# Kernel tuning notes

Hardware: AMD Instinct MI355X
Metric: run time of the kernel (lower is better)

The kernel has to match this reference:

```python
import jax, jax.numpy as jnp
import numpy as np

EPS = 1e-12  # clamp for sqrt stability in Gram-matrix distance

def _pairwise_euclid(X, Y):
    # [B,D],[M,D] -> [B,M] Euclidean distances via Gram trick (avoids [B,M,D] diff tensor)
    x2 = jnp.sum(X * X, axis=-1, keepdims=True)        # [B,1]
    y2 = jnp.sum(Y * Y, axis=-1)[None, :]              # [1,M]
    sq = x2 + y2 - 2.0 * (X @ Y.T)
    return jnp.sqrt(jnp.maximum(sq, EPS))

def setup_inputs() -> dict:
    key = jax.random.key(0)
    k1, k2, k3 = jax.random.split(key, 3)
    B, D = 4096, 128
    return {
        "rep_anchor": jax.random.normal(k1, (B, D), dtype=jnp.float32),
        "rep_pos": jax.random.normal(k2, (B, D), dtype=jnp.float32),
        "rep_neg": jax.random.normal(k3, (B, D), dtype=jnp.float32),
    }

def reference(rep_anchor, rep_pos, rep_neg):
    B = rep_anchor.shape[0]
    # distance_pos[i] = ||a_i - p_i||_2 (elementwise rows, like F.pairwise_distance)
    diff = rep_anchor - rep_pos
    distance_pos = jnp.sqrt(jnp.maximum(jnp.sum(diff * diff, axis=-1), EPS))  # [B]

    big = jnp.asarray(jnp.finfo(rep_anchor.dtype).max, rep_anchor.dtype)
    eye = jnp.eye(B, dtype=bool)
    # anchor-as-negative: exclude self (index i)
    d_aa = jnp.where(eye, big, _pairwise_euclid(rep_anchor, rep_anchor))  # [B,B]
    # pos-as-negative: rep_pos[i] is excluded for anchor i
    d_ap = jnp.where(eye, big, _pairwise_euclid(rep_anchor, rep_pos))    # [B,B]
    # all of rep_neg are negatives
    d_an = _pairwise_euclid(rep_anchor, rep_neg)                          # [B,B]

    hardest_neg = jnp.minimum(jnp.minimum(d_aa.min(axis=1), d_ap.min(axis=1)), d_an.min(axis=1))  # [B]
    # log1p(exp(x)) == softplus, computed stably
    loss_in_batch = jnp.logaddexp(0.0, distance_pos - hardest_neg)
    return jnp.mean(loss_in_batch)
```

## Files before the change

kernel.cpp:

```cpp
#include <hip/hip_runtime.h>
#include <math.h>

#define BDIM 4096
#define DDIM 128
#define EPSF 1e-12f
#define TI 128
#define TJ 64
#define NSPLIT 16
#define NSLICE (NSPLIT * 2)
#define ITILES (BDIM / TI)
#define JT 12
#define FLT_BIG 3.402823466e+38f
#define NCHUNK (16 * BDIM)

typedef __attribute__((ext_vector_type(8))) _Float16 f16x8;
typedef __attribute__((ext_vector_type(16))) float f32x16;

__device__ __forceinline__ void gload_lds16(const void* g, void* l) {
    __builtin_amdgcn_global_load_lds(
        (const __attribute__((address_space(1))) unsigned int*)(uintptr_t)g,
        (__attribute__((address_space(3))) unsigned int*)(unsigned int)(uintptr_t)l,
        16, 0, 0);
}

__device__ __forceinline__ unsigned int pack2h(float x, float y) {
    _Float16 hx = (_Float16)x, hy = (_Float16)y;
    unsigned short ux, uy;
    __builtin_memcpy(&ux, &hx, 2);
    __builtin_memcpy(&uy, &hy, 2);
    return (unsigned int)ux | ((unsigned int)uy << 16);
}

__global__ __launch_bounds__(256) void prep_kernel(
    const float* __restrict__ A, const float* __restrict__ P,
    const float* __restrict__ N, uint4* __restrict__ Xp,
    float* __restrict__ a2, float* __restrict__ p2,
    float* __restrict__ n2, float* __restrict__ dpos) {
    int gid = blockIdx.x * 256 + threadIdx.x;
    int sl = gid & 15;
    int row = gid >> 4;
    const float4 a0 = *(const float4*)&A[row * DDIM + sl * 8];
    const float4 a1 = *(const float4*)&A[row * DDIM + sl * 8 + 4];
    const float4 p0 = *(const float4*)&P[row * DDIM + sl * 8];
    const float4 p1 = *(const float4*)&P[row * DDIM + sl * 8 + 4];
    const float4 n0 = *(const float4*)&N[row * DDIM + sl * 8];
    const float4 n1 = *(const float4*)&N[row * DDIM + sl * 8 + 4];
    uint4 ca = {pack2h(a0.x, a0.y), pack2h(a0.z, a0.w),
                pack2h(a1.x, a1.y), pack2h(a1.z, a1.w)};
    uint4 cp = {pack2h(p0.x, p0.y), pack2h(p0.z, p0.w),
                pack2h(p1.x, p1.y), pack2h(p1.z, p1.w)};
    uint4 cn = {pack2h(n0.x, n0.y), pack2h(n0.z, n0.w),
                pack2h(n1.x, n1.y), pack2h(n1.z, n1.w)};
    Xp[(0 * 16 + sl) * BDIM + row] = ca;
    Xp[(1 * 16 + sl) * BDIM + row] = cp;
    Xp[(2 * 16 + sl) * BDIM + row] = cn;
    float sa = a0.x*a0.x + a0.y*a0.y + a0.z*a0.z + a0.w*a0.w
             + a1.x*a1.x + a1.y*a1.y + a1.z*a1.z + a1.w*a1.w;
    float sp = p0.x*p0.x + p0.y*p0.y + p0.z*p0.z + p0.w*p0.w
             + p1.x*p1.x + p1.y*p1.y + p1.z*p1.z + p1.w*p1.w;
    float sn = n0.x*n0.x + n0.y*n0.y + n0.z*n0.z + n0.w*n0.w
             + n1.x*n1.x + n1.y*n1.y + n1.z*n1.z + n1.w*n1.w;
    float d0 = a0.x-p0.x, d1 = a0.y-p0.y, d2 = a0.z-p0.z, d3 = a0.w-p0.w;
    float d4 = a1.x-p1.x, d5 = a1.y-p1.y, d6 = a1.z-p1.z, d7 = a1.w-p1.w;
    float sd = d0*d0 + d1*d1 + d2*d2 + d3*d3 + d4*d4 + d5*d5 + d6*d6 + d7*d7;
    #pragma unroll
    for (int off = 1; off < 16; off <<= 1) {
        sa += __shfl_xor(sa, off);
        sp += __shfl_xor(sp, off);
        sn += __shfl_xor(sn, off);
        sd += __shfl_xor(sd, off);
    }
    if (sl == 0) {
        a2[row] = sa;
        p2[row] = sp;
        n2[row] = sn;
        dpos[row] = sqrtf(fmaxf(sd, EPSF));
    }
}

__global__ __launch_bounds__(256, 2) void minsq_kernel(
    const ushort* __restrict__ Xp,
    const float* __restrict__ a2, const float* __restrict__ p2,
    const float* __restrict__ n2, float* __restrict__ partial) {
    __shared__ __align__(16) ushort pool[4][2][4096];

    const int tid = threadIdx.x;
    const int w = tid >> 6;
    const int lane = tid & 63;
    const int rg = w >> 1;
    const int ch = w & 1;
    const int iTile = blockIdx.x;
    const int split = blockIdx.y;
    const int i0 = iTile * TI;
    const int jt0 = split * JT;
    const int l31 = lane & 31;
    const int lhi = lane >> 5;
    ushort* const wbase = &pool[w][0][0];

    {
        int jt = jt0, m = jt >> 6, tc = jt & 63;
        int rowB = tc * TJ + ch * 32 + l31;
        #pragma unroll
        for (int k = 0; k < 8; ++k) {
            int slB = k * 2 + lhi;
            gload_lds16(Xp + (size_t)((m * 16 + slB) * BDIM + rowB) * 8,
                        wbase + k * 512);
        }
    }
    f16x8 a0[8], a1[8];
    {
        int rowA0 = i0 + rg * 64 + l31;
        #pragma unroll
        for (int t = 0; t < 8; ++t) {
            int slA = t * 2 + lhi;
            a0[t] = *(const f16x8*)(Xp + (size_t)(slA * BDIM + rowA0) * 8);
            a1[t] = *(const f16x8*)(Xp + (size_t)(slA * BDIM + rowA0 + 32) * 8);
        }
    }
    float y2h[JT];
    #pragma unroll
    for (int t = 0; t < JT; ++t) {
        int jt = jt0 + t, m = jt >> 6, tc = jt & 63;
        const float* y2g = (m == 0) ? a2 : ((m == 1) ? p2 : n2);
        y2h[t] = 0.5f * y2g[tc * TJ + ch * 32 + l31];
    }
    asm volatile("s_waitcnt vmcnt(0)" ::: "memory");
    __builtin_amdgcn_sched_barrier(0);

    float minv[2][16];
    #pragma unroll
    for (int rb = 0; rb < 2; ++rb)
        #pragma unroll
        for (int g = 0; g < 16; ++g) minv[rb][g] = FLT_BIG;

    #pragma unroll
    for (int idx = 0; idx < JT; ++idx) {
        if (idx + 1 < JT) {
            int jn = jt0 + idx + 1, mn = jn >> 6, tcn = jn & 63;
            int rowB = tcn * TJ + ch * 32 + l31;
            ushort* dst = wbase + ((idx + 1) & 1) * 4096;
            #pragma unroll
            for (int k = 0; k < 8; ++k) {
                int slB = k * 2 + lhi;
                gload_lds16(Xp + (size_t)((mn * 16 + slB) * BDIM + rowB) * 8,
                            dst + k * 512);
            }
            asm volatile("s_waitcnt vmcnt(8)" ::: "memory");
        } else {
            asm volatile("s_waitcnt vmcnt(0)" ::: "memory");
        }
        __builtin_amdgcn_sched_barrier(0);

        const ushort* buf = wbase + (idx & 1) * 4096;
        f32x16 acc0 = {}, acc1 = {};
        __builtin_amdgcn_s_setprio(1);
        #pragma unroll
        for (int t = 0; t < 8; ++t) {
            f16x8 b = *(const f16x8*)&buf[t * 512 + lane * 8];
            acc0 = __builtin_amdgcn_mfma_f32_32x32x16_f16(a0[t], b, acc0, 0, 0, 0);
            acc1 = __builtin_amdgcn_mfma_f32_32x32x16_f16(a1[t], b, acc1, 0, 0, 0);
        }
        __builtin_amdgcn_s_setprio(0);

        {
            int jt = jt0 + idx, m = jt >> 6, tc = jt & 63;
            float yh = y2h[idx];
            if (m < 2 && (tc >> 1) == iTile) {
                int jg = tc * TJ + ch * 32 + l31;
                #pragma unroll
                for (int rb = 0; rb < 2; ++rb) {
                    #pragma unroll
                    for (int g = 0; g < 16; ++g) {
                        int rloc = (g & 3) + 8 * (g >> 2) + 4 * lhi;
                        int ig = i0 + rg * 64 + rb * 32 + rloc;
                        float d = (rb == 0) ? acc0[g] : acc1[g];
                        float cand = yh - d;
                        if (ig == jg) cand = FLT_BIG;
                        minv[rb][g] = fminf(minv[rb][g], cand);
                    }
                }
            } else {
                #pragma unroll
                for (int g = 0; g < 16; ++g) {
                    minv[0][g] = fminf(minv[0][g], yh - acc0[g]);
                    minv[1][g] = fminf(minv[1][g], yh - acc1[g]);
                }
            }
        }
    }

    #pragma unroll
    for (int off = 1; off < 32; off <<= 1) {
        #pragma unroll
        for (int rb = 0; rb < 2; ++rb)
            #pragma unroll
            for (int g = 0; g < 16; ++g)
                minv[rb][g] = fminf(minv[rb][g], __shfl_xor(minv[rb][g], off));
    }
    if (l31 == 0) {
        int slice = split * 2 + ch;
        #pragma unroll
        for (int rb = 0; rb < 2; ++rb) {
            #pragma unroll
            for (int g = 0; g < 16; ++g) {
                int rloc = (g & 3) + 8 * (g >> 2) + 4 * lhi;
                int ig = i0 + rg * 64 + rb * 32 + rloc;
                partial[(size_t)ig * NSLICE + slice] = minv[rb][g];
            }
        }
    }
}

__global__ __launch_bounds__(256) void lossA_kernel(
    const float* __restrict__ partial, const float* __restrict__ a2,
    const float* __restrict__ dpos, float* __restrict__ bsum) {
    __shared__ float red[4];
    int i = blockIdx.x * 256 + threadIdx.x;
    const float4* pr = (const float4*)&partial[(size_t)i * NSLICE];
    float mv = FLT_BIG;
    #pragma unroll
    for (int q = 0; q < NSLICE / 4; ++q) {
        float4 v = pr[q];
        mv = fminf(mv, fminf(fminf(v.x, v.y), fminf(v.z, v.w)));
    }
    float h2 = a2[i] + 2.0f * mv;
    float hardest = sqrtf(fmaxf(h2, EPSF));
    float x = dpos[i] - hardest;
    float sum = fmaxf(x, 0.f) + log1pf(expf(-fabsf(x)));
    #pragma unroll
    for (int off = 32; off; off >>= 1) sum += __shfl_down(sum, off);
    if ((threadIdx.x & 63) == 0) red[threadIdx.x >> 6] = sum;
    __syncthreads();
    if (threadIdx.x == 0)
        bsum[blockIdx.x] = red[0] + red[1] + red[2] + red[3];
}

__global__ void lossB_kernel(const float* __restrict__ bsum,
                             float* __restrict__ out) {
    float v = (threadIdx.x < 16) ? bsum[threadIdx.x] : 0.f;
    #pragma unroll
    for (int off = 32; off; off >>= 1) v += __shfl_down(v, off);
    if (threadIdx.x == 0) out[0] = v * (1.0f / BDIM);
}

extern "C" void kernel_launch(void* const* d_in, const int* in_sizes, int n_in,
                              void* d_out, int out_size, void* d_ws, size_t ws_size,
                              hipStream_t stream) {
    const float* A = (const float*)d_in[0];
    const float* P = (const float*)d_in[1];
    const float* N = (const float*)d_in[2];

    float* ws = (float*)d_ws;
    float* a2 = ws;
    float* p2 = ws + BDIM;
    float* n2 = ws + 2 * BDIM;
    float* dpos = ws + 3 * BDIM;
    float* bsum = ws + 4 * BDIM;
    float* partial = ws + 4 * BDIM + 64;
    uint4* Xp = (uint4*)(partial + (size_t)BDIM * NSLICE);

    prep_kernel<<<256, 256, 0, stream>>>(A, P, N, Xp, a2, p2, n2, dpos);
    dim3 grid2(ITILES, NSPLIT);
    minsq_kernel<<<grid2, 256, 0, stream>>>((const ushort*)Xp, a2, p2, n2, partial);
    lossA_kernel<<<16, 256, 0, stream>>>(partial, a2, dpos, bsum);
    lossB_kernel<<<1, 64, 0, stream>>>(bsum, (float*)d_out);
}
```

Measured before the change: 36.00 us.

## Share block-wide LDS Y tile across waves and rebalance split grid

Each wave used to stage its own copy of the B tile in LDS. Now the four waves cooperatively load one shared double-buffered 64-row tile, with block barriers to keep the buffers in sync. This cuts redundant global-to-LDS traffic and LDS footprint in half, which should allow more resident blocks. The grid split also changes from 16 splits of 12 tiles to 24 splits of 8 tiles, giving more blocks but adding partial-min slices and per-iteration barrier costs.

```diff
diff --git a/kernel.cpp b/kernel.cpp
--- a/kernel.cpp
+++ b/kernel.cpp
@@ -6,12 +6,11 @@
 #define EPSF 1e-12f
 #define TI 128
 #define TJ 64
-#define NSPLIT 16
+#define NSPLIT 24
 #define NSLICE (NSPLIT * 2)
 #define ITILES (BDIM / TI)
-#define JT 12
+#define JT 8
 #define FLT_BIG 3.402823466e+38f
-#define NCHUNK (16 * BDIM)
 
 typedef __attribute__((ext_vector_type(8))) _Float16 f16x8;
 typedef __attribute__((ext_vector_type(16))) float f32x16;
@@ -82,131 +81,129 @@
     const ushort* __restrict__ Xp,
     const float* __restrict__ a2, const float* __restrict__ p2,
     const float* __restrict__ n2, float* __restrict__ partial) {
-    __shared__ __align__(16) ushort pool[4][2][4096];
+    __shared__ __align__(16) ushort Y[2][TJ * DDIM / 1];
 
     const int tid = threadIdx.x;
     const int w = tid >> 6;
     const int lane = tid & 63;
+    const int l31 = lane & 31;
+    const int lhi = lane >> 5;
     const int rg = w >> 1;
     const int ch = w & 1;
     const int iTile = blockIdx.x;
     const int split = blockIdx.y;
     const int i0 = iTile * TI;
     const int jt0 = split * JT;
-    const int l31 = lane & 31;
-    const int lhi = lane >> 5;
-    ushort* const wbase = &pool[w][0][0];
 
     {
-        int jt = jt0, m = jt >> 6, tc = jt & 63;
-        int rowB = tc * TJ + ch * 32 + l31;
-        #pragma unroll
-        for (int k = 0; k < 8; ++k) {
-            int slB = k * 2 + lhi;
-            gload_lds16(Xp + (size_t)((m * 16 + slB) * BDIM + rowB) * 8,
-                        wbase + k * 512);
+        int m = jt0 >> 6, tc = jt0 & 63;
+        #pragma unroll
+        for (int q = 0; q < 4; ++q) {
+            int sl = w * 4 + q;
+            gload_lds16(Xp + (size_t)((m * 16 + sl) * BDIM + tc * TJ + lane) * 8,
+                        (ushort*)&Y[0][0] + sl * 512);
         }
     }
     f16x8 a0[8], a1[8];
     {
-        int rowA0 = i0 + rg * 64 + l31;
+        int rowA = i0 + rg * 64 + l31;
         #pragma unroll
         for (int t = 0; t < 8; ++t) {
-            int slA = t * 2 + lhi;
-            a0[t] = *(const f16x8*)(Xp + (size_t)(slA * BDIM + rowA0) * 8);
-            a1[t] = *(const f16x8*)(Xp + (size_t)(slA * BDIM + rowA0 + 32) * 8);
-        }
-    }
-    float y2h[JT];
-    #pragma unroll
-    for (int t = 0; t < JT; ++t) {
-        int jt = jt0 + t, m = jt >> 6, tc = jt & 63;
+            int sl = t * 2 + lhi;
+            a0[t] = *(const f16x8*)(Xp + (size_t)(sl * BDIM + rowA) * 8);
+            a1[t] = *(const f16x8*)(Xp + (size_t)(sl * BDIM + rowA + 32) * 8);
+        }
+    }
+    float y2buf[2];
+    {
+        int m = jt0 >> 6, tc = jt0 & 63;
         const float* y2g = (m == 0) ? a2 : ((m == 1) ? p2 : n2);
-        y2h[t] = 0.5f * y2g[tc * TJ + ch * 32 + l31];
+        y2buf[0] = 0.5f * y2g[tc * TJ + ch * 32 + l31];
     }
     asm volatile("s_waitcnt vmcnt(0)" ::: "memory");
     __builtin_amdgcn_sched_barrier(0);
-
-    float minv[2][16];
-    #pragma unroll
-    for (int rb = 0; rb < 2; ++rb)
-        #pragma unroll
-        for (int g = 0; g < 16; ++g) minv[rb][g] = FLT_BIG;
-
-    #pragma unroll
-    for (int idx = 0; idx < JT; ++idx) {
-        if (idx + 1 < JT) {
-            int jn = jt0 + idx + 1, mn = jn >> 6, tcn = jn & 63;
-            int rowB = tcn * TJ + ch * 32 + l31;
-            ushort* dst = wbase + ((idx + 1) & 1) * 4096;
+    __builtin_amdgcn_s_barrier();
+    __builtin_amdgcn_sched_barrier(0);
+
+    float minv0[16], minv1[16];
+    #pragma unroll
+    for (int g = 0; g < 16; ++g) { minv0[g] = FLT_BIG; minv1[g] = FLT_BIG; }
+
+    #pragma unroll
+    for (int t = 0; t < JT; ++t) {
+        if (t + 1 < JT) {
+            int jn = jt0 + t + 1, mn = jn >> 6, tcn = jn & 63;
             #pragma unroll
-            for (int k = 0; k < 8; ++k) {
-                int slB = k * 2 + lhi;
-                gload_lds16(Xp + (size_t)((mn * 16 + slB) * BDIM + rowB) * 8,
-                            dst + k * 512);
+            for (int q = 0; q < 4; ++q) {
+                int sl = w * 4 + q;
+                gload_lds16(Xp + (size_t)((mn * 16 + sl) * BDIM + tcn * TJ + lane) * 8,
+                            (ushort*)&Y[(t + 1) & 1][0] + sl * 512);
             }
-            asm volatile("s_waitcnt vmcnt(8)" ::: "memory");
+            const float* y2g = (mn == 0) ? a2 : ((mn == 1) ? p2 : n2);
+            y2buf[(t + 1) & 1] = 0.5f * y2g[tcn * TJ + ch * 32 + l31];
+            asm volatile("s_waitcnt vmcnt(5)" ::: "memory");
         } else {
             asm volatile("s_waitcnt vmcnt(0)" ::: "memory");
         }
         __builtin_amdgcn_sched_barrier(0);
-
-        const ushort* buf = wbase + (idx & 1) * 4096;
+        __builtin_amdgcn_s_barrier();
+        __builtin_amdgcn_sched_barrier(0);
+
+        const ushort* buf = &Y[t & 1][0];
         f32x16 acc0 = {}, acc1 = {};
         __builtin_amdgcn_s_setprio(1);
         #pragma unroll
-        for (int t = 0; t < 8; ++t) {
-            f16x8 b = *(const f16x8*)&buf[t * 512 + lane * 8];
-            acc0 = __builtin_amdgcn_mfma_f32_32x32x16_f16(a0[t], b, acc0, 0, 0, 0);
-            acc1 = __builtin_amdgcn_mfma_f32_32x32x16_f16(a1[t], b, acc1, 0, 0, 0);
+        for (int k = 0; k < 8; ++k) {
+            int sl = k * 2 + lhi;
+            f16x8 b = *(const f16x8*)&buf[(sl * 64 + ch * 32 + l31) * 8];
+            acc0 = __builtin_amdgcn_mfma_f32_32x32x16_f16(a0[k], b, acc0, 0, 0, 0);
+            acc1 = __builtin_amdgcn_mfma_f32_32x32x16_f16(a1[k], b, acc1, 0, 0, 0);
         }
         __builtin_amdgcn_s_setprio(0);
 
         {
-            int jt = jt0 + idx, m = jt >> 6, tc = jt & 63;
-            float yh = y2h[idx];
+            int jt = jt0 + t, m = jt >> 6, tc = jt & 63;
+            float yh = y2buf[t & 1];
             if (m < 2 && (tc >> 1) == iTile) {
                 int jg = tc * TJ + ch * 32 + l31;
                 #pragma unroll
-                for (int rb = 0; rb < 2; ++rb) {
-                    #pragma unroll
-                    for (int g = 0; g < 16; ++g) {
-                        int rloc = (g & 3) + 8 * (g >> 2) + 4 * lhi;
-                        int ig = i0 + rg * 64 + rb * 32 + rloc;
-                        float d = (rb == 0) ? acc0[g] : acc1[g];
-                        float cand = yh - d;
-                        if (ig == jg) cand = FLT_BIG;
-                        minv[rb][g] = fminf(minv[rb][g], cand);
-                    }
+                for (int g = 0; g < 16; ++g) {
+                    int rloc = (g & 3) + 8 * (g >> 2) + 4 * lhi;
+                    int ig0 = i0 + rg * 64 + rloc;
+                    float c0 = yh - acc0[g];
+                    if (ig0 == jg) c0 = FLT_BIG;
+                    minv0[g] = fminf(minv0[g], c0);
+                    float c1 = yh - acc1[g];
+                    if (ig0 + 32 == jg) c1 = FLT_BIG;
+                    minv1[g] = fminf(minv1[g], c1);
                 }
             } else {
                 #pragma unroll
                 for (int g = 0; g < 16; ++g) {
-                    minv[0][g] = fminf(minv[0][g], yh - acc0[g]);
-                    minv[1][g] = fminf(minv[1][g], yh - acc1[g]);
+                    minv0[g] = fminf(minv0[g], yh - acc0[g]);
+                    minv1[g] = fminf(minv1[g], yh - acc1[g]);
                 }
             }
         }
+        __builtin_amdgcn_s_barrier();
     }
 
     #pragma unroll
     for (int off = 1; off < 32; off <<= 1) {
         #pragma unroll
-        for (int rb = 0; rb < 2; ++rb)
-            #pragma unroll
-            for (int g = 0; g < 16; ++g)
-                minv[rb][g] = fminf(minv[rb][g], __shfl_xor(minv[rb][g], off));
+        for (int g = 0; g < 16; ++g) {
+            minv0[g] = fminf(minv0[g], __shfl_xor(minv0[g], off));
+            minv1[g] = fminf(minv1[g], __shfl_xor(minv1[g], off));
+        }
     }
     if (l31 == 0) {
         int slice = split * 2 + ch;
         #pragma unroll
-        for (int rb = 0; rb < 2; ++rb) {
-            #pragma unroll
-            for (int g = 0; g < 16; ++g) {
-                int rloc = (g & 3) + 8 * (g >> 2) + 4 * lhi;
-                int ig = i0 + rg * 64 + rb * 32 + rloc;
-                partial[(size_t)ig * NSLICE + slice] = minv[rb][g];
-            }
+        for (int g = 0; g < 16; ++g) {
+            int rloc = (g & 3) + 8 * (g >> 2) + 4 * lhi;
+            int ig = i0 + rg * 64 + rloc;
+            partial[(size_t)ig * NSLICE + slice] = minv0[g];
+            partial[(size_t)(ig + 32) * NSLICE + slice] = minv1[g];
         }
     }
 }
```

After: 36.94 us. +2.6%, slower.

## Fold column norm bias into MFMA, shrink cross-lane reduction, widen loss reduction

Applied to the files above, without the earlier changes.

Each column's -0.5*||y||^2 is stored as a two-term fp16 split, so one extra MFMA per accumulator adds the bias directly. The epilogue becomes a plain running max with no per-element subtract. The in-wave shuffle reduction drops from 5 steps to 2, and more partial slices (256 per row) are written for the loss kernel to reduce wave-wide. The loss kernel now uses 64 blocks with one wave per row group. This trades per-element ALU and shuffle work for two extra MFMAs per tile and more partial-buffer traffic, and the fp16-split bias may slightly change precision.

```diff
diff --git a/kernel.cpp b/kernel.cpp
--- a/kernel.cpp
+++ b/kernel.cpp
@@ -7,14 +7,14 @@
 #define TI 128
 #define TJ 64
 #define NSPLIT 16
-#define NSLICE (NSPLIT * 2)
+#define NSLICE 256
 #define ITILES (BDIM / TI)
 #define JT 12
 #define FLT_BIG 3.402823466e+38f
-#define NCHUNK (16 * BDIM)
 
 typedef __attribute__((ext_vector_type(8))) _Float16 f16x8;
 typedef __attribute__((ext_vector_type(16))) float f32x16;
+union VU { uint4 u; f16x8 v; };
 
 __device__ __forceinline__ void gload_lds16(const void* g, void* l) {
     __builtin_amdgcn_global_load_lds(
@@ -34,8 +34,8 @@
 __global__ __launch_bounds__(256) void prep_kernel(
     const float* __restrict__ A, const float* __restrict__ P,
     const float* __restrict__ N, uint4* __restrict__ Xp,
-    float* __restrict__ a2, float* __restrict__ p2,
-    float* __restrict__ n2, float* __restrict__ dpos) {
+    unsigned int* __restrict__ y2c, float* __restrict__ a2,
+    float* __restrict__ dpos) {
     int gid = blockIdx.x * 256 + threadIdx.x;
     int sl = gid & 15;
     int row = gid >> 4;
@@ -72,33 +72,40 @@
     }
     if (sl == 0) {
         a2[row] = sa;
-        p2[row] = sp;
-        n2[row] = sn;
         dpos[row] = sqrtf(fmaxf(sd, EPSF));
+        float ya = 0.5f * sa, yp = 0.5f * sp, yn = 0.5f * sn;
+        float ha = (float)(_Float16)ya, hp = (float)(_Float16)yp,
+              hn = (float)(_Float16)yn;
+        y2c[0 * BDIM + row] = pack2h(-ha, -(ya - ha));
+        y2c[1 * BDIM + row] = pack2h(-hp, -(yp - hp));
+        y2c[2 * BDIM + row] = pack2h(-hn, -(yn - hn));
     }
 }
 
 __global__ __launch_bounds__(256, 2) void minsq_kernel(
-    const ushort* __restrict__ Xp,
-    const float* __restrict__ a2, const float* __restrict__ p2,
-    const float* __restrict__ n2, float* __restrict__ partial) {
+    const ushort* __restrict__ Xp, const unsigned int* __restrict__ y2c,
+    float* __restrict__ partial) {
     __shared__ __align__(16) ushort pool[4][2][4096];
 
     const int tid = threadIdx.x;
     const int w = tid >> 6;
     const int lane = tid & 63;
+    const int l31 = lane & 31;
+    const int lhi = lane >> 5;
     const int rg = w >> 1;
     const int ch = w & 1;
     const int iTile = blockIdx.x;
     const int split = blockIdx.y;
     const int i0 = iTile * TI;
     const int jt0 = split * JT;
-    const int l31 = lane & 31;
-    const int lhi = lane >> 5;
     ushort* const wbase = &pool[w][0][0];
 
+    VU au; au.u = (uint4){lhi == 0 ? 0x3C003C00u : 0u, 0u, 0u, 0u};
+    const f16x8 ax = au.v;
+
+    unsigned int yc_cur, yc_nxt;
     {
-        int jt = jt0, m = jt >> 6, tc = jt & 63;
+        int m = jt0 >> 6, tc = jt0 & 63;
         int rowB = tc * TJ + ch * 32 + l31;
         #pragma unroll
         for (int k = 0; k < 8; ++k) {
@@ -106,32 +113,24 @@
             gload_lds16(Xp + (size_t)((m * 16 + slB) * BDIM + rowB) * 8,
                         wbase + k * 512);
         }
+        yc_cur = y2c[m * BDIM + rowB];
     }
     f16x8 a0[8], a1[8];
     {
-        int rowA0 = i0 + rg * 64 + l31;
+        int rowA = i0 + rg * 64 + l31;
         #pragma unroll
         for (int t = 0; t < 8; ++t) {
             int slA = t * 2 + lhi;
-            a0[t] = *(const f16x8*)(Xp + (size_t)(slA * BDIM + rowA0) * 8);
-            a1[t] = *(const f16x8*)(Xp + (size_t)(slA * BDIM + rowA0 + 32) * 8);
-        }
-    }
-    float y2h[JT];
-    #pragma unroll
-    for (int t = 0; t < JT; ++t) {
-        int jt = jt0 + t, m = jt >> 6, tc = jt & 63;
-        const float* y2g = (m == 0) ? a2 : ((m == 1) ? p2 : n2);
-        y2h[t] = 0.5f * y2g[tc * TJ + ch * 32 + l31];
+            a0[t] = *(const f16x8*)(Xp + (size_t)(slA * BDIM + rowA) * 8);
+            a1[t] = *(const f16x8*)(Xp + (size_t)(slA * BDIM + rowA + 32) * 8);
+        }
     }
     asm volatile("s_waitcnt vmcnt(0)" ::: "memory");
     __builtin_amdgcn_sched_barrier(0);
 
-    float minv[2][16];
-    #pragma unroll
-    for (int rb = 0; rb < 2; ++rb)
-        #pragma unroll
-        for (int g = 0; g < 16; ++g) minv[rb][g] = FLT_BIG;
+    float maxv0[16], maxv1[16];
+    #pragma unroll
+    for (int g = 0; g < 16; ++g) { maxv0[g] = -FLT_BIG; maxv1[g] = -FLT_BIG; }
 
     #pragma unroll
     for (int idx = 0; idx < JT; ++idx) {
@@ -145,15 +144,22 @@
                 gload_lds16(Xp + (size_t)((mn * 16 + slB) * BDIM + rowB) * 8,
                             dst + k * 512);
             }
-            asm volatile("s_waitcnt vmcnt(8)" ::: "memory");
+            yc_nxt = y2c[mn * BDIM + rowB];
+            __builtin_amdgcn_sched_barrier(0);
+            asm volatile("s_waitcnt vmcnt(9)" ::: "memory");
         } else {
             asm volatile("s_waitcnt vmcnt(0)" ::: "memory");
         }
         __builtin_amdgcn_sched_barrier(0);
+
+        VU bu; bu.u = (uint4){yc_cur, 0u, 0u, 0u};
+        const f16x8 bx = bu.v;
 
         const ushort* buf = wbase + (idx & 1) * 4096;
         f32x16 acc0 = {}, acc1 = {};
         __builtin_amdgcn_s_setprio(1);
+        acc0 = __builtin_amdgcn_mfma_f32_32x32x16_f16(ax, bx, acc0, 0, 0, 0);
+        acc1 = __builtin_amdgcn_mfma_f32_32x32x16_f16(ax, bx, acc1, 0, 0, 0);
         #pragma unroll
         for (int t = 0; t < 8; ++t) {
             f16x8 b = *(const f16x8*)&buf[t * 512 + lane * 8];
@@ -161,52 +167,49 @@
             acc1 = __builtin_amdgcn_mfma_f32_32x32x16_f16(a1[t], b, acc1, 0, 0, 0);
         }
         __builtin_amdgcn_s_setprio(0);
+        yc_cur = yc_nxt;
 
         {
             int jt = jt0 + idx, m = jt >> 6, tc = jt & 63;
-            float yh = y2h[idx];
             if (m < 2 && (tc >> 1) == iTile) {
                 int jg = tc * TJ + ch * 32 + l31;
                 #pragma unroll
-                for (int rb = 0; rb < 2; ++rb) {
-                    #pragma unroll
-                    for (int g = 0; g < 16; ++g) {
-                        int rloc = (g & 3) + 8 * (g >> 2) + 4 * lhi;
-                        int ig = i0 + rg * 64 + rb * 32 + rloc;
-                        float d = (rb == 0) ? acc0[g] : acc1[g];
-                        float cand = yh - d;
-                        if (ig == jg) cand = FLT_BIG;
-                        minv[rb][g] = fminf(minv[rb][g], cand);
-                    }
+                for (int g = 0; g < 16; ++g) {
+                    int rloc = (g & 3) + 8 * (g >> 2) + 4 * lhi;
+                    int ig0 = i0 + rg * 64 + rloc;
+                    float c0 = acc0[g];
+                    if (ig0 == jg) c0 = -FLT_BIG;
+                    maxv0[g] = fmaxf(maxv0[g], c0);
+                    float c1 = acc1[g];
+                    if (ig0 + 32 == jg) c1 = -FLT_BIG;
+                    maxv1[g] = fmaxf(maxv1[g], c1);
                 }
             } else {
                 #pragma unroll
                 for (int g = 0; g < 16; ++g) {
-                    minv[0][g] = fminf(minv[0][g], yh - acc0[g]);
-                    minv[1][g] = fminf(minv[1][g], yh - acc1[g]);
+                    maxv0[g] = fmaxf(maxv0[g], acc0[g]);
+                    maxv1[g] = fmaxf(maxv1[g], acc1[g]);
                 }
             }
         }
     }
 
     #pragma unroll
-    for (int off = 1; off < 32; off <<= 1) {
-        #pragma unroll
-        for (int rb = 0; rb < 2; ++rb)
-            #pragma unroll
-            for (int g = 0; g < 16; ++g)
-                minv[rb][g] = fminf(minv[rb][g], __shfl_xor(minv[rb][g], off));
-    }
-    if (l31 == 0) {
-        int slice = split * 2 + ch;
-        #pragma unroll
-        for (int rb = 0; rb < 2; ++rb) {
-            #pragma unroll
-            for (int g = 0; g < 16; ++g) {
-                int rloc = (g & 3) + 8 * (g >> 2) + 4 * lhi;
-                int ig = i0 + rg * 64 + rb * 32 + rloc;
-                partial[(size_t)ig * NSLICE + slice] = minv[rb][g];
-            }
+    for (int off = 1; off < 4; off <<= 1) {
+        #pragma unroll
+        for (int g = 0; g < 16; ++g) {
+            maxv0[g] = fmaxf(maxv0[g], __shfl_xor(maxv0[g], off));
+            maxv1[g] = fmaxf(maxv1[g], __shfl_xor(maxv1[g], off));
+        }
+    }
+    if ((l31 & 3) == 0) {
+        int slice = (split * 2 + ch) * 8 + (l31 >> 2);
+        #pragma unroll
+        for (int g = 0; g < 16; ++g) {
+            int rloc = (g & 3) + 8 * (g >> 2) + 4 * lhi;
+            int ig = i0 + rg * 64 + rloc;
+            partial[(size_t)ig * NSLICE + slice] = maxv0[g];
+            partial[(size_t)(ig + 32) * NSLICE + slice] = maxv1[g];
         }
     }
 }
@@ -215,21 +218,25 @@
     const float* __restrict__ partial, const float* __restrict__ a2,
     const float* __restrict__ dpos, float* __restrict__ bsum) {
     __shared__ float red[4];
-    int i = blockIdx.x * 256 + threadIdx.x;
-    const float4* pr = (const float4*)&partial[(size_t)i * NSLICE];
-    float mv = FLT_BIG;
-    #pragma unroll
-    for (int q = 0; q < NSLICE / 4; ++q) {
-        float4 v = pr[q];
-        mv = fminf(mv, fminf(fminf(v.x, v.y), fminf(v.z, v.w)));
-    }
-    float h2 = a2[i] + 2.0f * mv;
-    float hardest = sqrtf(fmaxf(h2, EPSF));
-    float x = dpos[i] - hardest;
-    float sum = fmaxf(x, 0.f) + log1pf(expf(-fabsf(x)));
-    #pragma unroll
-    for (int off = 32; off; off >>= 1) sum += __shfl_down(sum, off);
-    if ((threadIdx.x & 63) == 0) red[threadIdx.x >> 6] = sum;
+    int w = threadIdx.x >> 6;
+    int lane = threadIdx.x & 63;
+    int wave = blockIdx.x * 4 + w;
+    float sum = 0.f;
+    #pragma unroll
+    for (int j = 0; j < 16; ++j) {
+        int row = wave + 256 * j;
+        float4 v = *(const float4*)&partial[(size_t)row * NSLICE + lane * 4];
+        float m = fmaxf(fmaxf(v.x, v.y), fmaxf(v.z, v.w));
+        #pragma unroll
+        for (int off = 32; off; off >>= 1) m = fmaxf(m, __shfl_xor(m, off));
+        if (lane == 0) {
+            float h2 = a2[row] - 2.0f * m;
+            float hardest = sqrtf(fmaxf(h2, EPSF));
+            float x = dpos[row] - hardest;
+            sum += fmaxf(x, 0.f) + log1pf(expf(-fabsf(x)));
+        }
+    }
+    if (lane == 0) red[w] = sum;
     __syncthreads();
     if (threadIdx.x == 0)
         bsum[blockIdx.x] = red[0] + red[1] + red[2] + red[3];
@@ -237,7 +244,7 @@
 
 __global__ void lossB_kernel(const float* __restrict__ bsum,
                              float* __restrict__ out) {
-    float v = (threadIdx.x < 16) ? bsum[threadIdx.x] : 0.f;
+    float v = bsum[threadIdx.x];
     #pragma unroll
     for (int off = 32; off; off >>= 1) v += __shfl_down(v, off);
     if (threadIdx.x == 0) out[0] = v * (1.0f / BDIM);
@@ -252,16 +259,15 @@
 
     float* ws = (float*)d_ws;
     float* a2 = ws;
-    float* p2 = ws + BDIM;
-    float* n2 = ws + 2 * BDIM;
-    float* dpos = ws + 3 * BDIM;
-    float* bsum = ws + 4 * BDIM;
-    float* partial = ws + 4 * BDIM + 64;
+    float* dpos = ws + BDIM;
+    unsigned int* y2c = (unsigned int*)(ws + 2 * BDIM);
+    float* bsum = ws + 5 * BDIM;
+    float* partial = ws + 5 * BDIM + 64;
     uint4* Xp = (uint4*)(partial + (size_t)BDIM * NSLICE);
 
-    prep_kernel<<<256, 256, 0, stream>>>(A, P, N, Xp, a2, p2, n2, dpos);
+    prep_kernel<<<256, 256, 0, stream>>>(A, P, N, Xp, y2c, a2, dpos);
     dim3 grid2(ITILES, NSPLIT);
-    minsq_kernel<<<grid2, 256, 0, stream>>>((const ushort*)Xp, a2, p2, n2, partial);
-    lossA_kernel<<<16, 256, 0, stream>>>(partial, a2, dpos, bsum);
+    minsq_kernel<<<grid2, 256, 0, stream>>>((const ushort*)Xp, y2c, partial);
+    lossA_kernel<<<64, 256, 0, stream>>>(partial, a2, dpos, bsum);
     lossB_kernel<<<1, 64, 0, stream>>>(bsum, (float*)d_out);
 }
```

Measured after the change: 58.64 us. +62.9%, slower.
